# Kernel optimization log

Hardware: AMD Instinct MI355X
Metric: run time of the kernel (lower is better)

Reference implementation:

```python
import jax, jax.numpy as jnp
import numpy as np

H = 16
EPS = 1e-5

def _layernorm(x, gamma, beta):
    mu = jnp.mean(x, axis=-1, keepdims=True)
    var = jnp.var(x, axis=-1, keepdims=True)
    return (x - mu) * jax.lax.rsqrt(var + EPS) * gamma + beta

def setup_inputs() -> dict:
    key = jax.random.key(0)
    ks = jax.random.split(key, 5)
    B, T, E = 4, 2048, 1024
    D = E // H
    return {
        "x": jax.random.normal(ks[0], (B, T, E), dtype=jnp.float32),
        "Wqkv": jax.random.normal(ks[1], (E, 3 * E), dtype=jnp.float32) * (E ** -0.5),
        "bqkv": jax.random.normal(ks[2], (3 * E,), dtype=jnp.float32) * 0.02,
        "q_gamma": jnp.ones((D,), jnp.float32),
        "q_beta": jnp.zeros((D,), jnp.float32),
        "k_gamma": jnp.ones((D,), jnp.float32),
        "k_beta": jnp.zeros((D,), jnp.float32),
        "Wproj": jax.random.normal(ks[3], (E, E), dtype=jnp.float32) * (E ** -0.5),
        "bproj": jnp.zeros((E,), jnp.float32),
    }

def reference(x, Wqkv, bqkv, q_gamma, q_beta, k_gamma, k_beta, Wproj, bproj):
    B, T, E = x.shape
    D = E // H
    qkv = x @ Wqkv + bqkv                      # [B,T,3E]
    q, k, v = jnp.split(qkv, 3, axis=-1)
    # b t (h d) -> b h t d
    to_heads = lambda a: a.reshape(B, T, H, D).transpose(0, 2, 1, 3)
    q, k, v = to_heads(q), to_heads(k), to_heads(v)
    q = _layernorm(q, q_gamma, q_beta)
    k = _layernorm(k, k_gamma, k_beta)
    scale = 1.0 / jnp.sqrt(jnp.float32(D))
    scores = jnp.einsum('bhtd,bhsd->bhts', q, k) * scale   # [B,H,T,T]
    attn = jax.nn.softmax(scores, axis=-1)
    y = jnp.einsum('bhts,bhsd->bhtd', attn, v)             # [B,H,T,D]
    y = y.transpose(0, 2, 1, 3).reshape(B, T, E)           # b h t d -> b t (h d)
    return y @ Wproj + bproj
```

## Files before the change

### kernel.cpp

```cpp
#include <hip/hip_runtime.h>

#define Hn  16
#define Dh  64
#define Bb  4
#define Tn  2048
#define En  1024
#define Mn  8192
#define N1  3072
#define Kn  1024
#define BHT (Bb*Hn*Tn)

typedef __attribute__((ext_vector_type(8)))  short  short8;
typedef __attribute__((ext_vector_type(4)))  short  short4v;
typedef __attribute__((ext_vector_type(4)))  float  f32x4;
typedef __attribute__((ext_vector_type(8)))  __bf16 bf16x8;

__device__ __forceinline__ float b2f(short s) {
  unsigned u = ((unsigned)(unsigned short)s) << 16;
  return __builtin_bit_cast(float, u);
}
__device__ __forceinline__ short f2b(float f) {
  unsigned u = __builtin_bit_cast(unsigned, f);
  u += 0x7fffu + ((u >> 16) & 1u);
  return (short)(u >> 16);
}
__device__ __forceinline__ f32x4 mfma16(short8 a, short8 b, f32x4 c) {
  return __builtin_amdgcn_mfma_f32_16x16x32_bf16(
      __builtin_bit_cast(bf16x8, a), __builtin_bit_cast(bf16x8, b), c, 0, 0, 0);
}
__device__ __forceinline__ void gload16(const void* g, void* l) {
  __builtin_amdgcn_global_load_lds(
      (const __attribute__((address_space(1))) unsigned int*)g,
      (__attribute__((address_space(3))) unsigned int*)l, 16, 0, 0);
}

__global__ __launch_bounds__(256) void cvt_x_kernel(const float* __restrict__ x,
                                                    short* __restrict__ xb) {
  const size_t i = ((size_t)blockIdx.x * 256 + threadIdx.x) * 8;
  f32x4 a = *(const f32x4*)&x[i];
  f32x4 b = *(const f32x4*)&x[i + 4];
  short8 o;
  o[0]=f2b(a[0]); o[1]=f2b(a[1]); o[2]=f2b(a[2]); o[3]=f2b(a[3]);
  o[4]=f2b(b[0]); o[5]=f2b(b[1]); o[6]=f2b(b[2]); o[7]=f2b(b[3]);
  *(short8*)&xb[i] = o;
}

__global__ __launch_bounds__(256) void transpose_w_kernel(const float* __restrict__ in,
                                                          short* __restrict__ out,
                                                          int R, int C) {
  __shared__ float tile[32][33];
  const int tid = threadIdx.x;
  const int c0 = blockIdx.x * 32, r0 = blockIdx.y * 32;
  const int lr = tid >> 3, lc = (tid & 7) * 4;
  f32x4 v = *(const f32x4*)&in[(size_t)(r0 + lr) * C + c0 + lc];
  tile[lr][lc] = v[0]; tile[lr][lc+1] = v[1]; tile[lr][lc+2] = v[2]; tile[lr][lc+3] = v[3];
  __syncthreads();
  const int oc = tid >> 3, orr = (tid & 7) * 4;
  short4v ov;
  ov[0] = f2b(tile[orr][oc]);   ov[1] = f2b(tile[orr+1][oc]);
  ov[2] = f2b(tile[orr+2][oc]); ov[3] = f2b(tile[orr+3][oc]);
  *(short4v*)&out[(size_t)(c0 + oc) * R + r0 + orr] = ov;
}

template<int MODE>
__global__ __launch_bounds__(256) void gemm_kernel(
    const short* __restrict__ A, const short* __restrict__ Bt,
    const float* __restrict__ bias, float* __restrict__ Cf,
    short* __restrict__ qo, short* __restrict__ ko2, short* __restrict__ vo,
    const float* __restrict__ qg, const float* __restrict__ qb,
    const float* __restrict__ kg, const float* __restrict__ kb,
    int N, int NBX, int cpx) {
  __shared__ short As[4096];
  __shared__ short Bs[4096];
  const int lin = blockIdx.x;
  const int swz = (lin & 7) * cpx + (lin >> 3);
  const int bx = swz % NBX, by = swz / NBX;
  const int tid = threadIdx.x, lane = tid & 63, w = tid >> 6;
  const int rowBase = by * 128, colBase = bx * 128;
  f32x4 acc[4][4] = {};
  const int srow = tid >> 2, sk = (tid & 3) << 3;
  const short* Ag = A  + (size_t)(rowBase + srow) * Kn + sk;
  const short* Bg = Bt + (size_t)(colBase + srow) * Kn + sk;
  short* AsW = As + w * 512;
  short* BsW = Bs + w * 512;
  const int ar = (w >> 1) * 64, bc = (w & 1) * 64;
  const int lg8 = (lane >> 4) * 8, lr = lane & 15;

  for (int kt = 0; kt < Kn; kt += 32) {
    __syncthreads();
    gload16(Ag + kt,            AsW);
    gload16(Ag + kt + 64 * Kn,  AsW + 2048);
    gload16(Bg + kt,            BsW);
    gload16(Bg + kt + 64 * Kn,  BsW + 2048);
    __syncthreads();
    short8 af[4], bfr[4];
#pragma unroll
    for (int m = 0; m < 4; ++m) af[m]  = *(const short8*)&As[(ar + m*16 + lr)*32 + lg8];
#pragma unroll
    for (int n = 0; n < 4; ++n) bfr[n] = *(const short8*)&Bs[(bc + n*16 + lr)*32 + lg8];
#pragma unroll
    for (int m = 0; m < 4; ++m)
#pragma unroll
      for (int n = 0; n < 4; ++n)
        acc[m][n] = mfma16(af[m], bfr[n], acc[m][n]);
  }

  const int gr0 = rowBase + ar + (lane >> 4) * 4;
  const int gc0 = colBase + bc + lr;

  float bb[4];
#pragma unroll
  for (int n = 0; n < 4; ++n) bb[n] = bias[gc0 + n * 16];
#pragma unroll
  for (int m = 0; m < 4; ++m)
#pragma unroll
    for (int n = 0; n < 4; ++n)
#pragma unroll
      for (int r = 0; r < 4; ++r) acc[m][n][r] += bb[n];

  if (MODE == 1) {
    const int which = colBase >> 10;
    if (which < 2) {
      const float* gp = (which == 0) ? qg : kg;
      const float* bp = (which == 0) ? qb : kb;
      const float sc = (which == 0) ? 0.1803368801111204f : 1.0f;
      float gam[4], bet[4];
#pragma unroll
      for (int n = 0; n < 4; ++n) { gam[n] = gp[n * 16 + lr]; bet[n] = bp[n * 16 + lr]; }
#pragma unroll
      for (int m = 0; m < 4; ++m)
#pragma unroll
        for (int r = 0; r < 4; ++r) {
          float s1 = 0.f, s2 = 0.f;
#pragma unroll
          for (int n = 0; n < 4; ++n) {
            const float v = acc[m][n][r];
            s1 += v; s2 += v * v;
          }
#pragma unroll
          for (int off = 1; off < 16; off <<= 1) {
            s1 += __shfl_xor(s1, off);
            s2 += __shfl_xor(s2, off);
          }
          const float mu = s1 * 0.015625f;
          const float rs = rsqrtf(s2 * 0.015625f - mu * mu + 1e-5f);
#pragma unroll
          for (int n = 0; n < 4; ++n)
            acc[m][n][r] = ((acc[m][n][r] - mu) * rs * gam[n] + bet[n]) * sc;
        }
    }
  }

#pragma unroll
  for (int m = 0; m < 4; ++m) {
#pragma unroll
    for (int n = 0; n < 4; ++n) {
      const int gc = gc0 + n * 16;
#pragma unroll
      for (int r = 0; r < 4; ++r) {
        const int gr = gr0 + m * 16 + r;
        const float v = acc[m][n][r];
        if (MODE == 0) {
          Cf[(size_t)gr * N + gc] = v;
        } else {
          const int which = gc >> 10, e = gc & 1023;
          const int hh = e >> 6, d = e & 63;
          const int bidx = gr >> 11, t = gr & 2047;
          const int bh = bidx * Hn + hh;
          if (which == 0) {
            qo[((size_t)bh * Tn + t) * Dh + d] = f2b(v);
          } else if (which == 1) {
            ko2[((size_t)bh * Tn + t) * Dh + d] = f2b(v);
          } else {
            vo[((size_t)bh * Dh + d) * Tn + t] = f2b(v);
          }
        }
      }
    }
  }
}

__global__ __launch_bounds__(256) void flash_kernel(
    const short* __restrict__ qp, const short* __restrict__ kp,
    const short* __restrict__ vt, short* __restrict__ y) {
  __shared__ short Ks[2][4096];
  __shared__ short Vs[2][4096];
  __shared__ short Ps[4096];
  const int tid = threadIdx.x, lane = tid & 63, w = tid >> 6;
  const int lr = lane & 15, lg = lane >> 4;

  const int j0 = blockIdx.x;
  const int xcd = j0 & 7, kk0 = j0 >> 3;
  const int bh = 8 * xcd + (kk0 & 7), qt = kk0 >> 3;

  const int qrow0 = qt * 128 + w * 32;
  const short* qbase = qp + ((size_t)bh * Tn + qrow0) * Dh;

  short8 aq[2][2];
#pragma unroll
  for (int m = 0; m < 2; ++m)
#pragma unroll
    for (int kk = 0; kk < 2; ++kk)
      aq[m][kk] = *(const short8*)&qbase[(m*16 + lr)*64 + kk*32 + lg*8];

  short8 ones;
#pragma unroll
  for (int i = 0; i < 8; ++i) ones[i] = (short)0x3F80;

  f32x4 o[2][4] = {};
  f32x4 lacc[2] = {};
  float mrow[2][4];
#pragma unroll
  for (int m = 0; m < 2; ++m)
#pragma unroll
    for (int r = 0; r < 4; ++r) mrow[m][r] = -3e38f;

  const int srow = tid >> 3;
  const int sc = (tid & 7) * 8;
  short* Pw = Ps + w * 1024;
  const short* kb = kp + (size_t)bh * Tn * Dh;
  const short* vb = vt + (size_t)bh * Dh * Tn;

#define STAGE(jt, bsel)                                                   \
  {                                                                       \
    _Pragma("unroll")                                                     \
    for (int i = 0; i < 2; ++i) {                                         \
      const int row = i * 32 + srow;                                      \
      const int scs = sc ^ ((row & 7) << 3);                              \
      gload16(kb + (size_t)((jt) * 64 + row) * Dh + scs,                  \
              &Ks[bsel][w * 512 + i * 2048]);                             \
      gload16(vb + (size_t)row * Tn + (jt) * 64 + scs,                    \
              &Vs[bsel][w * 512 + i * 2048]);                             \
    }                                                                     \
  }

#define PSW(q) ((((q) & 3) << 3) ^ (((q) & 4) << 2))

  STAGE(0, 0);
  __syncthreads();

  for (int j = 0; j < Tn / 64; ++j) {
    const int cur = j & 1;
    if (j + 1 < Tn / 64) STAGE(j + 1, cur ^ 1);

    short8 bk[4][2];
#pragma unroll
    for (int n = 0; n < 4; ++n)
#pragma unroll
      for (int kk = 0; kk < 2; ++kk) {
        const int row = n * 16 + lr;
        bk[n][kk] = *(const short8*)&Ks[cur][row*64 + ((kk*32 + lg*8) ^ ((row & 7) << 3))];
      }
    f32x4 s[2][4] = {};
    __builtin_amdgcn_s_setprio(1);
#pragma unroll
    for (int m = 0; m < 2; ++m)
#pragma unroll
      for (int n = 0; n < 4; ++n) {
        s[m][n] = mfma16(aq[m][0], bk[n][0], s[m][n]);
        s[m][n] = mfma16(aq[m][1], bk[n][1], s[m][n]);
      }
    __builtin_amdgcn_s_setprio(0);

    float pm[2][4];
#pragma unroll
    for (int m = 0; m < 2; ++m)
#pragma unroll
      for (int r = 0; r < 4; ++r)
        pm[m][r] = fmaxf(fmaxf(s[m][0][r], s[m][1][r]), fmaxf(s[m][2][r], s[m][3][r]));
    int ok = 1;
#pragma unroll
    for (int m = 0; m < 2; ++m)
#pragma unroll
      for (int r = 0; r < 4; ++r)
        ok &= (pm[m][r] <= mrow[m][r] + 11.0f) ? 1 : 0;
    if (!__all(ok)) {
      float tm[2][4];
#pragma unroll
      for (int m = 0; m < 2; ++m)
#pragma unroll
        for (int r = 0; r < 4; ++r) tm[m][r] = pm[m][r];
#pragma unroll
      for (int off = 1; off < 16; off <<= 1)
#pragma unroll
        for (int m = 0; m < 2; ++m)
#pragma unroll
          for (int r = 0; r < 4; ++r)
            tm[m][r] = fmaxf(tm[m][r], __shfl_xor(tm[m][r], off));
#pragma unroll
      for (int m = 0; m < 2; ++m)
#pragma unroll
        for (int r = 0; r < 4; ++r) {
          const float mn = fmaxf(mrow[m][r], tm[m][r]);
          const float corr = __builtin_amdgcn_exp2f(mrow[m][r] - mn);
          lacc[m][r] *= corr;
#pragma unroll
          for (int dn = 0; dn < 4; ++dn) o[m][dn][r] *= corr;
          mrow[m][r] = mn;
        }
    }

    short8 bv[4][2];
#pragma unroll
    for (int dn = 0; dn < 4; ++dn)
#pragma unroll
      for (int kk = 0; kk < 2; ++kk) {
        const int row = dn * 16 + lr;
        bv[dn][kk] = *(const short8*)&Vs[cur][row*64 + ((kk*32 + lg*8) ^ ((row & 7) << 3))];
      }

#pragma unroll
    for (int m = 0; m < 2; ++m)
#pragma unroll
      for (int n = 0; n < 2; ++n)
#pragma unroll
        for (int r = 0; r < 4; ++r) {
          const float p = __builtin_amdgcn_exp2f(s[m][n][r] - mrow[m][r]);
          const unsigned u = __builtin_bit_cast(unsigned, p);
          const int q = m*16 + lg*4 + r;
          Pw[q*32 + ((n*16 + lr) ^ PSW(q))] = (short)(u >> 16);
        }
    short8 pa0[2];
#pragma unroll
    for (int m = 0; m < 2; ++m) {
      const int q = m*16 + lr;
      pa0[m] = *(const short8*)&Pw[q*32 + ((lg*8) ^ PSW(q))];
    }
    __builtin_amdgcn_s_setprio(1);
#pragma unroll
    for (int m = 0; m < 2; ++m) {
      lacc[m] = mfma16(pa0[m], ones, lacc[m]);
#pragma unroll
      for (int dn = 0; dn < 4; ++dn)
        o[m][dn] = mfma16(pa0[m], bv[dn][0], o[m][dn]);
    }
    __builtin_amdgcn_s_setprio(0);

#pragma unroll
    for (int m = 0; m < 2; ++m)
#pragma unroll
      for (int n = 0; n < 2; ++n)
#pragma unroll
        for (int r = 0; r < 4; ++r) {
          const float p = __builtin_amdgcn_exp2f(s[m][2 + n][r] - mrow[m][r]);
          const unsigned u = __builtin_bit_cast(unsigned, p);
          const int q = m*16 + lg*4 + r;
          Pw[q*32 + ((n*16 + lr) ^ PSW(q))] = (short)(u >> 16);
        }
    short8 pa1[2];
#pragma unroll
    for (int m = 0; m < 2; ++m) {
      const int q = m*16 + lr;
      pa1[m] = *(const short8*)&Pw[q*32 + ((lg*8) ^ PSW(q))];
    }
    __builtin_amdgcn_s_setprio(1);
#pragma unroll
    for (int m = 0; m < 2; ++m) {
      lacc[m] = mfma16(pa1[m], ones, lacc[m]);
#pragma unroll
      for (int dn = 0; dn < 4; ++dn)
        o[m][dn] = mfma16(pa1[m], bv[dn][1], o[m][dn]);
    }
    __builtin_amdgcn_s_setprio(0);

    __syncthreads();
  }
#undef STAGE
#undef PSW

  const int b = bh >> 4, hh = bh & 15;
  short* yb = y + (size_t)b * Tn * En + hh * 64;
#pragma unroll
  for (int m = 0; m < 2; ++m)
#pragma unroll
    for (int r = 0; r < 4; ++r) {
      const float rl = 1.0f / lacc[m][r];
      const int t = qrow0 + m*16 + lg*4 + r;
#pragma unroll
      for (int dn = 0; dn < 4; ++dn) {
        const int d = dn*16 + lr;
        yb[(size_t)t * En + d] = f2b(o[m][dn][r] * rl);
      }
    }
}

extern "C" void kernel_launch(void* const* d_in, const int* in_sizes, int n_in,
                              void* d_out, int out_size, void* d_ws, size_t ws_size,
                              hipStream_t stream) {
  const float* x     = (const float*)d_in[0];
  const float* Wqkv  = (const float*)d_in[1];
  const float* bqkv  = (const float*)d_in[2];
  const float* qg    = (const float*)d_in[3];
  const float* qb    = (const float*)d_in[4];
  const float* kg    = (const float*)d_in[5];
  const float* kb    = (const float*)d_in[6];
  const float* Wproj = (const float*)d_in[7];
  const float* bproj = (const float*)d_in[8];
  float* out = (float*)d_out;

  char* p = (char*)d_ws;
  short* xb     = (short*)p; p += (size_t)Mn * Kn * 2;
  short* wqkvT  = (short*)p; p += (size_t)N1 * Kn * 2;
  short* wprojT = (short*)p; p += (size_t)En * Kn * 2;
  short* qp     = (short*)p; p += (size_t)Mn * Kn * 2;
  short* kp     = (short*)p; p += (size_t)Mn * Kn * 2;
  short* vtb    = (short*)p; p += (size_t)Mn * Kn * 2;
  short* yb     = (short*)p; p += (size_t)Mn * Kn * 2;

  cvt_x_kernel<<<Mn * Kn / (256 * 8), 256, 0, stream>>>(x, xb);
  transpose_w_kernel<<<dim3(N1 / 32, Kn / 32), 256, 0, stream>>>(Wqkv, wqkvT, Kn, N1);
  transpose_w_kernel<<<dim3(En / 32, Kn / 32), 256, 0, stream>>>(Wproj, wprojT, Kn, En);
  gemm_kernel<1><<<(N1 / 128) * (Mn / 128), 256, 0, stream>>>(
      xb, wqkvT, bqkv, nullptr, qp, kp, vtb, qg, qb, kg, kb,
      N1, N1 / 128, (N1 / 128) * (Mn / 128) / 8);
  flash_kernel<<<1024, 256, 0, stream>>>(qp, kp, vtb, yb);
  gemm_kernel<0><<<(En / 128) * (Mn / 128), 256, 0, stream>>>(
      yb, wprojT, bproj, out, nullptr, nullptr, nullptr, nullptr, nullptr, nullptr, nullptr,
      En, En / 128, (En / 128) * (Mn / 128) / 8);
}
```

Baseline: 264.5 us.

## Double per-wave query rows in flash kernel and process keys in halves

Each wave now handles 64 query rows instead of 32, so a block covers 256 rows. This halves the grid to 512 blocks and doubles how much each loaded K/V tile is reused. The 64-key tile is processed as two 32-key halves, each with its own online-softmax max update and PV MFMA pass, which limits the size of the live score registers. In exchange, the larger accumulators raise register pressure, the fewer blocks lower occupancy and parallelism across CUs, and the P scratch in shared memory doubles.

```diff
diff --git a/kernel.cpp b/kernel.cpp
--- a/kernel.cpp
+++ b/kernel.cpp
@@ -185,7 +185,7 @@
     const short* __restrict__ vt, short* __restrict__ y) {
   __shared__ short Ks[2][4096];
   __shared__ short Vs[2][4096];
-  __shared__ short Ps[4096];
+  __shared__ short Ps[8192];
   const int tid = threadIdx.x, lane = tid & 63, w = tid >> 6;
   const int lr = lane & 15, lg = lane >> 4;
 
@@ -193,12 +193,12 @@
   const int xcd = j0 & 7, kk0 = j0 >> 3;
   const int bh = 8 * xcd + (kk0 & 7), qt = kk0 >> 3;
 
-  const int qrow0 = qt * 128 + w * 32;
+  const int qrow0 = qt * 256 + w * 64;
   const short* qbase = qp + ((size_t)bh * Tn + qrow0) * Dh;
 
-  short8 aq[2][2];
-#pragma unroll
-  for (int m = 0; m < 2; ++m)
+  short8 aq[4][2];
+#pragma unroll
+  for (int m = 0; m < 4; ++m)
 #pragma unroll
     for (int kk = 0; kk < 2; ++kk)
       aq[m][kk] = *(const short8*)&qbase[(m*16 + lr)*64 + kk*32 + lg*8];
@@ -207,17 +207,17 @@
 #pragma unroll
   for (int i = 0; i < 8; ++i) ones[i] = (short)0x3F80;
 
-  f32x4 o[2][4] = {};
-  f32x4 lacc[2] = {};
-  float mrow[2][4];
-#pragma unroll
-  for (int m = 0; m < 2; ++m)
+  f32x4 o[4][4] = {};
+  f32x4 lacc[4] = {};
+  float mrow[4][4];
+#pragma unroll
+  for (int m = 0; m < 4; ++m)
 #pragma unroll
     for (int r = 0; r < 4; ++r) mrow[m][r] = -3e38f;
 
   const int srow = tid >> 3;
   const int sc = (tid & 7) * 8;
-  short* Pw = Ps + w * 1024;
+  short* Pw = Ps + w * 2048;
   const short* kb = kp + (size_t)bh * Tn * Dh;
   const short* vb = vt + (size_t)bh * Dh * Tn;
 
@@ -243,125 +243,94 @@
     const int cur = j & 1;
     if (j + 1 < Tn / 64) STAGE(j + 1, cur ^ 1);
 
-    short8 bk[4][2];
-#pragma unroll
-    for (int n = 0; n < 4; ++n)
-#pragma unroll
-      for (int kk = 0; kk < 2; ++kk) {
-        const int row = n * 16 + lr;
-        bk[n][kk] = *(const short8*)&Ks[cur][row*64 + ((kk*32 + lg*8) ^ ((row & 7) << 3))];
-      }
-    f32x4 s[2][4] = {};
-    __builtin_amdgcn_s_setprio(1);
-#pragma unroll
-    for (int m = 0; m < 2; ++m)
-#pragma unroll
-      for (int n = 0; n < 4; ++n) {
-        s[m][n] = mfma16(aq[m][0], bk[n][0], s[m][n]);
-        s[m][n] = mfma16(aq[m][1], bk[n][1], s[m][n]);
-      }
-    __builtin_amdgcn_s_setprio(0);
-
-    float pm[2][4];
-#pragma unroll
-    for (int m = 0; m < 2; ++m)
-#pragma unroll
-      for (int r = 0; r < 4; ++r)
-        pm[m][r] = fmaxf(fmaxf(s[m][0][r], s[m][1][r]), fmaxf(s[m][2][r], s[m][3][r]));
-    int ok = 1;
-#pragma unroll
-    for (int m = 0; m < 2; ++m)
-#pragma unroll
-      for (int r = 0; r < 4; ++r)
-        ok &= (pm[m][r] <= mrow[m][r] + 11.0f) ? 1 : 0;
-    if (!__all(ok)) {
-      float tm[2][4];
-#pragma unroll
-      for (int m = 0; m < 2; ++m)
-#pragma unroll
-        for (int r = 0; r < 4; ++r) tm[m][r] = pm[m][r];
-#pragma unroll
-      for (int off = 1; off < 16; off <<= 1)
-#pragma unroll
-        for (int m = 0; m < 2; ++m)
-#pragma unroll
-          for (int r = 0; r < 4; ++r)
-            tm[m][r] = fmaxf(tm[m][r], __shfl_xor(tm[m][r], off));
-#pragma unroll
-      for (int m = 0; m < 2; ++m)
-#pragma unroll
-        for (int r = 0; r < 4; ++r) {
-          const float mn = fmaxf(mrow[m][r], tm[m][r]);
-          const float corr = __builtin_amdgcn_exp2f(mrow[m][r] - mn);
-          lacc[m][r] *= corr;
-#pragma unroll
-          for (int dn = 0; dn < 4; ++dn) o[m][dn][r] *= corr;
-          mrow[m][r] = mn;
+#pragma unroll
+    for (int half = 0; half < 2; ++half) {
+      short8 bk[2][2];
+#pragma unroll
+      for (int n = 0; n < 2; ++n)
+#pragma unroll
+        for (int kk = 0; kk < 2; ++kk) {
+          const int row = (half * 2 + n) * 16 + lr;
+          bk[n][kk] = *(const short8*)&Ks[cur][row*64 + ((kk*32 + lg*8) ^ ((row & 7) << 3))];
         }
+      f32x4 s[4][2] = {};
+      __builtin_amdgcn_s_setprio(1);
+#pragma unroll
+      for (int m = 0; m < 4; ++m)
+#pragma unroll
+        for (int n = 0; n < 2; ++n) {
+          s[m][n] = mfma16(aq[m][0], bk[n][0], s[m][n]);
+          s[m][n] = mfma16(aq[m][1], bk[n][1], s[m][n]);
+        }
+      __builtin_amdgcn_s_setprio(0);
+
+      float pm[4][4];
+#pragma unroll
+      for (int m = 0; m < 4; ++m)
+#pragma unroll
+        for (int r = 0; r < 4; ++r)
+          pm[m][r] = fmaxf(s[m][0][r], s[m][1][r]);
+      int ok = 1;
+#pragma unroll
+      for (int m = 0; m < 4; ++m)
+#pragma unroll
+        for (int r = 0; r < 4; ++r)
+          ok &= (pm[m][r] <= mrow[m][r] + 11.0f) ? 1 : 0;
+      if (!__all(ok)) {
+#pragma unroll
+        for (int off = 1; off < 16; off <<= 1)
+#pragma unroll
+          for (int m = 0; m < 4; ++m)
+#pragma unroll
+            for (int r = 0; r < 4; ++r)
+              pm[m][r] = fmaxf(pm[m][r], __shfl_xor(pm[m][r], off));
+#pragma unroll
+        for (int m = 0; m < 4; ++m)
+#pragma unroll
+          for (int r = 0; r < 4; ++r) {
+            const float mn = fmaxf(mrow[m][r], pm[m][r]);
+            const float corr = __builtin_amdgcn_exp2f(mrow[m][r] - mn);
+            lacc[m][r] *= corr;
+#pragma unroll
+            for (int dn = 0; dn < 4; ++dn) o[m][dn][r] *= corr;
+            mrow[m][r] = mn;
+          }
+      }
+
+#pragma unroll
+      for (int m = 0; m < 4; ++m)
+#pragma unroll
+        for (int n = 0; n < 2; ++n)
+#pragma unroll
+          for (int r = 0; r < 4; ++r) {
+            const float p = __builtin_amdgcn_exp2f(s[m][n][r] - mrow[m][r]);
+            const unsigned u = __builtin_bit_cast(unsigned, p);
+            const int q = m*16 + lg*4 + r;
+            Pw[q*32 + ((n*16 + lr) ^ PSW(q))] = (short)(u >> 16);
+          }
+
+      short8 pa[4];
+#pragma unroll
+      for (int m = 0; m < 4; ++m) {
+        const int q = m*16 + lr;
+        pa[m] = *(const short8*)&Pw[q*32 + ((lg*8) ^ PSW(q))];
+      }
+      short8 bv[4];
+#pragma unroll
+      for (int dn = 0; dn < 4; ++dn) {
+        const int row = dn * 16 + lr;
+        bv[dn] = *(const short8*)&Vs[cur][row*64 + ((half*32 + lg*8) ^ ((row & 7) << 3))];
+      }
+      __builtin_amdgcn_s_setprio(1);
+#pragma unroll
+      for (int m = 0; m < 4; ++m) {
+        lacc[m] = mfma16(pa[m], ones, lacc[m]);
+#pragma unroll
+        for (int dn = 0; dn < 4; ++dn)
+          o[m][dn] = mfma16(pa[m], bv[dn], o[m][dn]);
+      }
+      __builtin_amdgcn_s_setprio(0);
     }
-
-    short8 bv[4][2];
-#pragma unroll
-    for (int dn = 0; dn < 4; ++dn)
-#pragma unroll
-      for (int kk = 0; kk < 2; ++kk) {
-        const int row = dn * 16 + lr;
-        bv[dn][kk] = *(const short8*)&Vs[cur][row*64 + ((kk*32 + lg*8) ^ ((row & 7) << 3))];
-      }
-
-#pragma unroll
-    for (int m = 0; m < 2; ++m)
-#pragma unroll
-      for (int n = 0; n < 2; ++n)
-#pragma unroll
-        for (int r = 0; r < 4; ++r) {
-          const float p = __builtin_amdgcn_exp2f(s[m][n][r] - mrow[m][r]);
-          const unsigned u = __builtin_bit_cast(unsigned, p);
-          const int q = m*16 + lg*4 + r;
-          Pw[q*32 + ((n*16 + lr) ^ PSW(q))] = (short)(u >> 16);
-        }
-    short8 pa0[2];
-#pragma unroll
-    for (int m = 0; m < 2; ++m) {
-      const int q = m*16 + lr;
-      pa0[m] = *(const short8*)&Pw[q*32 + ((lg*8) ^ PSW(q))];
-    }
-    __builtin_amdgcn_s_setprio(1);
-#pragma unroll
-    for (int m = 0; m < 2; ++m) {
-      lacc[m] = mfma16(pa0[m], ones, lacc[m]);
-#pragma unroll
-      for (int dn = 0; dn < 4; ++dn)
-        o[m][dn] = mfma16(pa0[m], bv[dn][0], o[m][dn]);
-    }
-    __builtin_amdgcn_s_setprio(0);
-
-#pragma unroll
-    for (int m = 0; m < 2; ++m)
-#pragma unroll
-      for (int n = 0; n < 2; ++n)
-#pragma unroll
-        for (int r = 0; r < 4; ++r) {
-          const float p = __builtin_amdgcn_exp2f(s[m][2 + n][r] - mrow[m][r]);
-          const unsigned u = __builtin_bit_cast(unsigned, p);
-          const int q = m*16 + lg*4 + r;
-          Pw[q*32 + ((n*16 + lr) ^ PSW(q))] = (short)(u >> 16);
-        }
-    short8 pa1[2];
-#pragma unroll
-    for (int m = 0; m < 2; ++m) {
-      const int q = m*16 + lr;
-      pa1[m] = *(const short8*)&Pw[q*32 + ((lg*8) ^ PSW(q))];
-    }
-    __builtin_amdgcn_s_setprio(1);
-#pragma unroll
-    for (int m = 0; m < 2; ++m) {
-      lacc[m] = mfma16(pa1[m], ones, lacc[m]);
-#pragma unroll
-      for (int dn = 0; dn < 4; ++dn)
-        o[m][dn] = mfma16(pa1[m], bv[dn][1], o[m][dn]);
-    }
-    __builtin_amdgcn_s_setprio(0);
 
     __syncthreads();
   }
@@ -371,7 +340,7 @@
   const int b = bh >> 4, hh = bh & 15;
   short* yb = y + (size_t)b * Tn * En + hh * 64;
 #pragma unroll
-  for (int m = 0; m < 2; ++m)
+  for (int m = 0; m < 4; ++m)
 #pragma unroll
     for (int r = 0; r < 4; ++r) {
       const float rl = 1.0f / lacc[m][r];
@@ -413,7 +382,7 @@
   gemm_kernel<1><<<(N1 / 128) * (Mn / 128), 256, 0, stream>>>(
       xb, wqkvT, bqkv, nullptr, qp, kp, vtb, qg, qb, kg, kb,
       N1, N1 / 128, (N1 / 128) * (Mn / 128) / 8);
-  flash_kernel<<<1024, 256, 0, stream>>>(qp, kp, vtb, yb);
+  flash_kernel<<<512, 256, 0, stream>>>(qp, kp, vtb, yb);
   gemm_kernel<0><<<(En / 128) * (Mn / 128), 256, 0, stream>>>(
       yb, wprojT, bproj, out, nullptr, nullptr, nullptr, nullptr, nullptr, nullptr, nullptr,
       En, En / 128, (En / 128) * (Mn / 128) / 8);
```

Result: slower. 309.7 us (+17.1%).

## Double-buffer GEMM LDS tiles and load V fragments directly from global in flash kernel

Applied to the files above, without the earlier changes.

The GEMM main loop now uses two LDS buffers, prefetching the next K tile while computing on the current one. This removes one barrier per iteration and lets global loads overlap the MFMAs. In the attention kernel, V is no longer staged through shared memory; each wave loads its V^T fragments straight from global memory into registers at the start of each iteration. That cuts LDS use and traffic, but V is now read redundantly by every wave and global latency sits on the critical path.

```diff
diff --git a/kernel.cpp b/kernel.cpp
--- a/kernel.cpp
+++ b/kernel.cpp
@@ -70,8 +70,8 @@
     const float* __restrict__ qg, const float* __restrict__ qb,
     const float* __restrict__ kg, const float* __restrict__ kb,
     int N, int NBX, int cpx) {
-  __shared__ short As[4096];
-  __shared__ short Bs[4096];
+  __shared__ short As[2][4096];
+  __shared__ short Bs[2][4096];
   const int lin = blockIdx.x;
   const int swz = (lin & 7) * cpx + (lin >> 3);
   const int bx = swz % NBX, by = swz / NBX;
@@ -81,29 +81,36 @@
   const int srow = tid >> 2, sk = (tid & 3) << 3;
   const short* Ag = A  + (size_t)(rowBase + srow) * Kn + sk;
   const short* Bg = Bt + (size_t)(colBase + srow) * Kn + sk;
-  short* AsW = As + w * 512;
-  short* BsW = Bs + w * 512;
   const int ar = (w >> 1) * 64, bc = (w & 1) * 64;
   const int lg8 = (lane >> 4) * 8, lr = lane & 15;
 
-  for (int kt = 0; kt < Kn; kt += 32) {
-    __syncthreads();
-    gload16(Ag + kt,            AsW);
-    gload16(Ag + kt + 64 * Kn,  AsW + 2048);
-    gload16(Bg + kt,            BsW);
-    gload16(Bg + kt + 64 * Kn,  BsW + 2048);
-    __syncthreads();
+#define GSTAGE(kt, b)                                    \
+  {                                                      \
+    gload16(Ag + (kt),           &As[b][w * 512]);       \
+    gload16(Ag + (kt) + 64 * Kn, &As[b][w * 512 + 2048]);\
+    gload16(Bg + (kt),           &Bs[b][w * 512]);       \
+    gload16(Bg + (kt) + 64 * Kn, &Bs[b][w * 512 + 2048]);\
+  }
+
+  GSTAGE(0, 0);
+  __syncthreads();
+
+  for (int it = 0; it < Kn / 32; ++it) {
+    const int cur = it & 1;
+    if (it + 1 < Kn / 32) GSTAGE((it + 1) * 32, cur ^ 1);
     short8 af[4], bfr[4];
 #pragma unroll
-    for (int m = 0; m < 4; ++m) af[m]  = *(const short8*)&As[(ar + m*16 + lr)*32 + lg8];
-#pragma unroll
-    for (int n = 0; n < 4; ++n) bfr[n] = *(const short8*)&Bs[(bc + n*16 + lr)*32 + lg8];
+    for (int m = 0; m < 4; ++m) af[m]  = *(const short8*)&As[cur][(ar + m*16 + lr)*32 + lg8];
+#pragma unroll
+    for (int n = 0; n < 4; ++n) bfr[n] = *(const short8*)&Bs[cur][(bc + n*16 + lr)*32 + lg8];
 #pragma unroll
     for (int m = 0; m < 4; ++m)
 #pragma unroll
       for (int n = 0; n < 4; ++n)
         acc[m][n] = mfma16(af[m], bfr[n], acc[m][n]);
-  }
+    __syncthreads();
+  }
+#undef GSTAGE
 
   const int gr0 = rowBase + ar + (lane >> 4) * 4;
   const int gc0 = colBase + bc + lr;
@@ -184,7 +191,6 @@
     const short* __restrict__ qp, const short* __restrict__ kp,
     const short* __restrict__ vt, short* __restrict__ y) {
   __shared__ short Ks[2][4096];
-  __shared__ short Vs[2][4096];
   __shared__ short Ps[4096];
   const int tid = threadIdx.x, lane = tid & 63, w = tid >> 6;
   const int lr = lane & 15, lg = lane >> 4;
@@ -229,8 +235,6 @@
       const int scs = sc ^ ((row & 7) << 3);                              \
       gload16(kb + (size_t)((jt) * 64 + row) * Dh + scs,                  \
               &Ks[bsel][w * 512 + i * 2048]);                             \
-      gload16(vb + (size_t)row * Tn + (jt) * 64 + scs,                    \
-              &Vs[bsel][w * 512 + i * 2048]);                             \
     }                                                                     \
   }
 
@@ -241,6 +245,15 @@
 
   for (int j = 0; j < Tn / 64; ++j) {
     const int cur = j & 1;
+
+    const short* vbj = vb + j * 64;
+    short8 bv[4][2];
+#pragma unroll
+    for (int dn = 0; dn < 4; ++dn)
+#pragma unroll
+      for (int kk = 0; kk < 2; ++kk)
+        bv[dn][kk] = *(const short8*)&vbj[(size_t)(dn*16 + lr) * Tn + kk*32 + lg*8];
+
     if (j + 1 < Tn / 64) STAGE(j + 1, cur ^ 1);
 
     short8 bk[4][2];
@@ -299,15 +312,6 @@
           mrow[m][r] = mn;
         }
     }
-
-    short8 bv[4][2];
-#pragma unroll
-    for (int dn = 0; dn < 4; ++dn)
-#pragma unroll
-      for (int kk = 0; kk < 2; ++kk) {
-        const int row = dn * 16 + lr;
-        bv[dn][kk] = *(const short8*)&Vs[cur][row*64 + ((kk*32 + lg*8) ^ ((row & 7) << 3))];
-      }
 
 #pragma unroll
     for (int m = 0; m < 2; ++m)
```

Result: slower. 436.1 us (+64.9%).
